# Performance work log

Measured on AMD Instinct MI355X. Metric: run time of the kernel, lower is better.

The kernel has to match this reference:

```python
import jax, jax.numpy as jnp
import numpy as np

N_FUNS = 10  # subset of SYMBOLIC_LIB safe on all of R

def _apply_funs(z, fun_ids):
    # z: (batch, out, in); fun_ids: (out, in) int ids selecting the symbolic fn
    branches = [
        z,                      # 0: 'x'
        z * z,                  # 1: 'x^2'
        z * z * z,              # 2: 'x^3'
        jnp.sin(z),             # 3: 'sin'
        jnp.tanh(z),            # 4: 'tanh'
        jax.nn.sigmoid(z),      # 5: 'sigmoid'
        jnp.exp(-z * z),        # 6: 'gaussian'
        jnp.abs(z),             # 7: 'abs'
        jnp.arctan(z),          # 8: 'arctan'
        jnp.exp(z),             # 9: 'exp'
    ]
    ids = fun_ids[None, :, :]  # broadcast over batch
    return jnp.select([ids == k for k in range(N_FUNS)], branches)


def setup_inputs() -> dict:
    key = jax.random.key(0)
    k1, k2, k3 = jax.random.split(key, 3)
    batch, in_f, out_f = 4096, 128, 128
    x = jax.random.normal(k1, (batch, in_f), dtype=jnp.float32)
    affine = jax.random.normal(k2, (out_f, in_f, 4), dtype=jnp.float32)
    mask = jnp.eye(in_f, dtype=jnp.float32)  # default buffer: identity
    fun_ids = jax.random.randint(k3, (out_f, in_f), 0, N_FUNS, dtype=jnp.int32)
    return {"x": x, "affine": affine, "mask": mask, "fun_ids": fun_ids}


def reference(x, affine, mask, fun_ids):
    # reduce inputs through the mask (identity by default): (batch, reduced_in)
    x_red = jnp.einsum("bi,ri->br", x, mask)
    a = affine[None, :, :, 0]  # (1, out, in)
    b = affine[None, :, :, 1]
    c = affine[None, :, :, 2]
    d = affine[None, :, :, 3]
    z = a * x_red[:, None, :] + b          # (batch, out, in)
    postacts = c * _apply_funs(z, fun_ids) + d  # (batch, out, in)
    y = jnp.sum(postacts, axis=2)           # (batch, out)
    return y, postacts
```

## Files before the change

### kernel.cpp

```cpp
#include <hip/hip_runtime.h>
#include <cmath>

#define XR_BB   16
#define OGROUP  8
#define BCHUNK  16

__global__ __launch_bounds__(256) void xred_kernel(const float* __restrict__ x,
                                                   const float* __restrict__ mask,
                                                   float* __restrict__ xred) {
    __shared__ float ms[128][129];
    __shared__ float xs[128][20];
    const int tid   = threadIdx.x;
    const int bbase = blockIdx.x * XR_BB;

    const float4* m4 = (const float4*)mask;
    for (int k = tid; k < 4096; k += 256) {
        float4 v = m4[k];
        int row = k >> 5;
        int col = (k & 31) * 4;
        ms[row][col]     = v.x;
        ms[row][col + 1] = v.y;
        ms[row][col + 2] = v.z;
        ms[row][col + 3] = v.w;
    }
    for (int k = tid; k < XR_BB * 128; k += 256) {
        int b = k >> 7, i = k & 127;
        xs[i][b] = x[(size_t)(bbase + b) * 128 + i];
    }
    __syncthreads();

    const int r = tid & 127;
    const int g = tid >> 7;
    float acc[8] = {0.f, 0.f, 0.f, 0.f, 0.f, 0.f, 0.f, 0.f};
    for (int i = 0; i < 128; ++i) {
        const float  m  = ms[r][i];
        const float4 xa = *(const float4*)&xs[i][8 * g];
        const float4 xb = *(const float4*)&xs[i][8 * g + 4];
        acc[0] += m * xa.x; acc[1] += m * xa.y; acc[2] += m * xa.z; acc[3] += m * xa.w;
        acc[4] += m * xb.x; acc[5] += m * xb.y; acc[6] += m * xb.z; acc[7] += m * xb.w;
    }
    #pragma unroll
    for (int j = 0; j < 8; ++j)
        xred[(size_t)(bbase + 8 * g + j) * 128 + r] = acc[j];
}

__global__ __launch_bounds__(256, 4) void kan_main(const float4* __restrict__ xred4,
                                                   const float4* __restrict__ affine,
                                                   const int* __restrict__ fun_ids,
                                                   float* __restrict__ y,
                                                   float4* __restrict__ post4) {
    const int tid = threadIdx.x;
    const int oo  = tid >> 5;
    const int il  = tid & 31;
    const int o   = blockIdx.x * OGROUP + oo;

    float4 A[4]; int f[4];
    #pragma unroll
    for (int j = 0; j < 4; ++j) {
        A[j] = affine[(size_t)o * 128 + il * 4 + j];
        f[j] = fun_ids[(size_t)o * 128 + il * 4 + j];
    }

    bool m1[4], m2[4], m3[4], m7[4], m8[4], me[4];
    float k1[4], k2[4], An[4], Bn[4], Dd[4];
    #pragma unroll
    for (int j = 0; j < 4; ++j) {
        const int fj = f[j];
        m1[j] = (fj == 1); m2[j] = (fj == 2); m3[j] = (fj == 3);
        m7[j] = (fj == 7); m8[j] = (fj == 8);
        me[j] = (fj >= 4 && fj <= 6) || (fj == 9);
        float k1v = 0.f, k2v = 0.f, Anv = 0.f, Bnv = 1.f, Ddv = 0.f;
        if      (fj == 4) { k1v = -2.f; Anv = 1.f; Bnv = -1.f; Ddv = 1.f; }
        else if (fj == 5) { k1v = -1.f; Anv = 1.f; Bnv =  0.f; Ddv = 1.f; }
        else if (fj == 6) { k2v = -1.f; }
        else if (fj == 9) { k1v =  1.f; }
        k1[j] = k1v; k2[j] = k2v; An[j] = Anv; Bn[j] = Bnv; Dd[j] = Ddv;
    }

    const int b0 = blockIdx.y * BCHUNK;

    for (int bb = 0; bb < BCHUNK; ++bb) {
        const int b = b0 + bb;
        const float4 xr = xred4[(size_t)b * 32 + il];
        const float xv[4] = {xr.x, xr.y, xr.z, xr.w};

        float p[4];
        #pragma unroll
        for (int j = 0; j < 4; ++j) {
            const float z  = fmaf(A[j].x, xv[j], A[j].y);
            const float zz = z * z;
            float pv = m1[j] ? zz : z;
            pv = m2[j] ? zz * z : pv;
            pv = m7[j] ? fabsf(z) : pv;
            const float s = __sinf(z);
            pv = m3[j] ? s : pv;
            const float arg = fminf(fmaf(k2[j], zz, k1[j] * z), 80.f);
            const float e   = __expf(arg);
            const float num = fmaf(Bn[j], e, An[j]);
            const float den = fmaf(Dd[j], e, 1.0f);
            const float r   = num * __builtin_amdgcn_rcpf(den);
            pv = me[j] ? r : pv;
            const float az  = fabsf(z);
            const bool  big = az > 1.0f;
            const float t   = big ? __builtin_amdgcn_rcpf(az) : az;
            const float t2  = t * t;
            float q = fmaf(t2, -0.01172120f, 0.05265332f);
            q = fmaf(t2, q, -0.11643287f);
            q = fmaf(t2, q,  0.19354346f);
            q = fmaf(t2, q, -0.33262347f);
            q = fmaf(t2, q,  0.99997726f);
            q = t * q;
            q = big ? 1.57079632679f - q : q;
            const float at = copysignf(q, z);
            pv = m8[j] ? at : pv;
            p[j] = fmaf(A[j].z, pv, A[j].w);
        }

        post4[((size_t)b * 128 + o) * 32 + il] = make_float4(p[0], p[1], p[2], p[3]);

        float s = (p[0] + p[1]) + (p[2] + p[3]);
        s += __shfl_xor(s, 1, 64);
        s += __shfl_xor(s, 2, 64);
        s += __shfl_xor(s, 4, 64);
        s += __shfl_xor(s, 8, 64);
        s += __shfl_xor(s, 16, 64);
        if (il == 0) y[(size_t)b * 128 + o] = s;
    }
}

extern "C" void kernel_launch(void* const* d_in, const int* in_sizes, int n_in,
                              void* d_out, int out_size, void* d_ws, size_t ws_size,
                              hipStream_t stream) {
    const float* x       = (const float*)d_in[0];
    const float* affine  = (const float*)d_in[1];
    const float* mask    = (const float*)d_in[2];
    const int*   fun_ids = (const int*)d_in[3];

    const int batch = in_sizes[0] / 128;

    float* xred     = (float*)d_ws;
    float* y        = (float*)d_out;
    float* postacts = y + (size_t)batch * 128;

    xred_kernel<<<dim3(batch / XR_BB), dim3(256), 0, stream>>>(x, mask, xred);

    kan_main<<<dim3(128 / OGROUP, batch / BCHUNK), dim3(256), 0, stream>>>(
        (const float4*)xred, (const float4*)affine, fun_ids, y, (float4*)postacts);
}
```

Measured before the change: 301.4 us.

## Retile mask reduction, prefetch xred, shorten arctan polynomial, use nontemporal stores

The mask-reduction kernel is retiled so each block loads only a 32-row slice of the mask against 32 batch rows, giving a 2D grid with a smaller shared-memory footprint. The main kernel drops the occupancy hint from its launch bounds, prefetches the next batch row of xred one iteration ahead, and writes postacts and y with nontemporal stores to limit cache pollution from the large output stream. It also swaps the degree-11 arctan polynomial for a degree-5 one, which removes FMAs but lowers arctan accuracy and may exceed tolerance.

Result: no change. 306.3 us (+1.6%).

```diff
diff --git a/kernel.cpp b/kernel.cpp
--- a/kernel.cpp
+++ b/kernel.cpp
@@ -1,20 +1,24 @@
 #include <hip/hip_runtime.h>
 #include <cmath>
 
-#define XR_BB   16
+#define XR_RT   32
+#define XR_BC   32
 #define OGROUP  8
 #define BCHUNK  16
+
+typedef float nfloat4 __attribute__((ext_vector_type(4)));
 
 __global__ __launch_bounds__(256) void xred_kernel(const float* __restrict__ x,
                                                    const float* __restrict__ mask,
                                                    float* __restrict__ xred) {
-    __shared__ float ms[128][129];
-    __shared__ float xs[128][20];
-    const int tid   = threadIdx.x;
-    const int bbase = blockIdx.x * XR_BB;
+    __shared__ float ms[XR_RT][129];
+    __shared__ float xs[128][40];
+    const int tid = threadIdx.x;
+    const int r0  = blockIdx.x * XR_RT;
+    const int b0  = blockIdx.y * XR_BC;
 
-    const float4* m4 = (const float4*)mask;
-    for (int k = tid; k < 4096; k += 256) {
+    const float4* m4 = (const float4*)(mask + (size_t)r0 * 128);
+    for (int k = tid; k < XR_RT * 32; k += 256) {
         float4 v = m4[k];
         int row = k >> 5;
         int col = (k & 31) * 4;
@@ -23,32 +27,30 @@
         ms[row][col + 2] = v.z;
         ms[row][col + 3] = v.w;
     }
-    for (int k = tid; k < XR_BB * 128; k += 256) {
+    for (int k = tid; k < XR_BC * 128; k += 256) {
         int b = k >> 7, i = k & 127;
-        xs[i][b] = x[(size_t)(bbase + b) * 128 + i];
+        xs[i][b] = x[(size_t)(b0 + b) * 128 + i];
     }
     __syncthreads();
 
-    const int r = tid & 127;
-    const int g = tid >> 7;
-    float acc[8] = {0.f, 0.f, 0.f, 0.f, 0.f, 0.f, 0.f, 0.f};
+    const int r = tid & 31;
+    const int g = tid >> 5;
+    float acc[4] = {0.f, 0.f, 0.f, 0.f};
     for (int i = 0; i < 128; ++i) {
         const float  m  = ms[r][i];
-        const float4 xa = *(const float4*)&xs[i][8 * g];
-        const float4 xb = *(const float4*)&xs[i][8 * g + 4];
+        const float4 xa = *(const float4*)&xs[i][4 * g];
         acc[0] += m * xa.x; acc[1] += m * xa.y; acc[2] += m * xa.z; acc[3] += m * xa.w;
-        acc[4] += m * xb.x; acc[5] += m * xb.y; acc[6] += m * xb.z; acc[7] += m * xb.w;
     }
     #pragma unroll
-    for (int j = 0; j < 8; ++j)
-        xred[(size_t)(bbase + 8 * g + j) * 128 + r] = acc[j];
+    for (int j = 0; j < 4; ++j)
+        xred[(size_t)(b0 + 4 * g + j) * 128 + (r0 + r)] = acc[j];
 }
 
-__global__ __launch_bounds__(256, 4) void kan_main(const float4* __restrict__ xred4,
-                                                   const float4* __restrict__ affine,
-                                                   const int* __restrict__ fun_ids,
-                                                   float* __restrict__ y,
-                                                   float4* __restrict__ post4) {
+__global__ __launch_bounds__(256) void kan_main(const float4* __restrict__ xred4,
+                                                const float4* __restrict__ affine,
+                                                const int* __restrict__ fun_ids,
+                                                float* __restrict__ y,
+                                                float4* __restrict__ post4) {
     const int tid = threadIdx.x;
     const int oo  = tid >> 5;
     const int il  = tid & 31;
@@ -79,9 +81,14 @@
 
     const int b0 = blockIdx.y * BCHUNK;
 
+    float4 xr = xred4[(size_t)b0 * 32 + il];
+
+    #pragma unroll 2
     for (int bb = 0; bb < BCHUNK; ++bb) {
         const int b = b0 + bb;
-        const float4 xr = xred4[(size_t)b * 32 + il];
+        float4 xr_n = xr;
+        if (bb + 1 < BCHUNK) xr_n = xred4[(size_t)(b + 1) * 32 + il];
+
         const float xv[4] = {xr.x, xr.y, xr.z, xr.w};
 
         float p[4];
@@ -104,11 +111,8 @@
             const bool  big = az > 1.0f;
             const float t   = big ? __builtin_amdgcn_rcpf(az) : az;
             const float t2  = t * t;
-            float q = fmaf(t2, -0.01172120f, 0.05265332f);
-            q = fmaf(t2, q, -0.11643287f);
-            q = fmaf(t2, q,  0.19354346f);
-            q = fmaf(t2, q, -0.33262347f);
-            q = fmaf(t2, q,  0.99997726f);
+            float q = fmaf(t2, 0.079331f, -0.288679f);
+            q = fmaf(t2, q, 0.995354f);
             q = t * q;
             q = big ? 1.57079632679f - q : q;
             const float at = copysignf(q, z);
@@ -116,7 +120,9 @@
             p[j] = fmaf(A[j].z, pv, A[j].w);
         }
 
-        post4[((size_t)b * 128 + o) * 32 + il] = make_float4(p[0], p[1], p[2], p[3]);
+        nfloat4 pv4 = {p[0], p[1], p[2], p[3]};
+        __builtin_nontemporal_store(pv4,
+            reinterpret_cast<nfloat4*>(&post4[((size_t)b * 128 + o) * 32 + il]));
 
         float s = (p[0] + p[1]) + (p[2] + p[3]);
         s += __shfl_xor(s, 1, 64);
@@ -124,7 +130,9 @@
         s += __shfl_xor(s, 4, 64);
         s += __shfl_xor(s, 8, 64);
         s += __shfl_xor(s, 16, 64);
-        if (il == 0) y[(size_t)b * 128 + o] = s;
+        if (il == 0) __builtin_nontemporal_store(s, &y[(size_t)b * 128 + o]);
+
+        xr = xr_n;
     }
 }
 
@@ -142,7 +150,7 @@
     float* y        = (float*)d_out;
     float* postacts = y + (size_t)batch * 128;
 
-    xred_kernel<<<dim3(batch / XR_BB), dim3(256), 0, stream>>>(x, mask, xred);
+    xred_kernel<<<dim3(128 / XR_RT, batch / XR_BC), dim3(256), 0, stream>>>(x, mask, xred);
 
     kan_main<<<dim3(128 / OGROUP, batch / BCHUNK), dim3(256), 0, stream>>>(
         (const float4*)xred, (const float4*)affine, fun_ids, y, (float4*)postacts);
```
